# Performance work log

Measured on AMD Instinct MI355X. Metric: run time of the kernel, lower is better.

## Reference

```python
import jax, jax.numpy as jnp
import numpy as np

B, L, D = 4, 4096, 1024
H, M = 16, 256
DH = D // H  # 64


def setup_inputs() -> dict:
    key = jax.random.key(0)
    ks = jax.random.split(key, 7)
    s = 1.0 / np.sqrt(D).astype(np.float32)  # keep activations O(1) so exp() stays sane
    x = jax.random.normal(ks[0], (B, L, D), dtype=jnp.float32)
    Wq = jax.random.normal(ks[1], (D, D), dtype=jnp.float32) * s
    Wk = jax.random.normal(ks[2], (D, D), dtype=jnp.float32) * s
    Wv = jax.random.normal(ks[3], (D, D), dtype=jnp.float32) * s
    Wo = jax.random.normal(ks[4], (D, D), dtype=jnp.float32) * s
    bo = jnp.zeros((D,), dtype=jnp.float32)
    omega = jax.random.normal(ks[5], (DH, M), dtype=jnp.float32)
    return {"x": x, "Wq": Wq, "Wk": Wk, "Wv": Wv, "Wo": Wo, "bo": bo, "omega": omega}


def _phi(x, omega):
    # x: (B,H,L,dh) -> positive random features (B,H,L,m)
    scale = DH ** 0.25
    x_s = x / scale
    proj = jnp.einsum('bhld,dm->bhlm', x_s, omega)
    norm_sq = jnp.sum(x_s * x_s, axis=-1, keepdims=True) * 0.5
    return jnp.exp(proj - norm_sq) / (M ** 0.5)


def reference(x, Wq, Wk, Wv, Wo, bo, omega):
    # nn.Linear: y = x @ W.T
    def heads(W):
        return (x @ W.T).reshape(B, L, H, DH).transpose(0, 2, 1, 3)
    Q, K, V = heads(Wq), heads(Wk), heads(Wv)
    Q_feat = _phi(Q, omega)   # (B,H,L,m)
    K_feat = _phi(K, omega)   # (B,H,L,m)
    KV = jnp.einsum('bhlm,bhld->bhmd', K_feat, V)      # (B,H,m,dh)
    out = jnp.einsum('bhlm,bhmd->bhld', Q_feat, KV)    # (B,H,L,dh)
    K_sum = K_feat.sum(axis=2)                          # (B,H,m)
    norm = jnp.einsum('bhlm,bhm->bhl', Q_feat, K_sum)
    norm = jnp.clip(norm, 1e-6, None)[..., None]
    out = out / norm
    out = out.transpose(0, 2, 1, 3).reshape(B, L, D)
    return out @ Wo.T + bo
```

## Files before the change

### kernel.cpp

```cpp
#include <hip/hip_runtime.h>

typedef unsigned short u16;
typedef __attribute__((ext_vector_type(4))) float f32x4;
typedef _Float16 f16x8 __attribute__((ext_vector_type(8)));
typedef __attribute__((ext_vector_type(4))) u16   u16x4;
typedef __attribute__((ext_vector_type(8))) u16   u16x8;

#define DEV static __device__ __forceinline__

constexpr int Ll = 4096;

DEV float h2f(u16 v) { _Float16 h; __builtin_memcpy(&h, &v, 2); return (float)h; }
DEV u16 f2h(float f) { _Float16 h = (_Float16)f; u16 u; __builtin_memcpy(&u, &h, 2); return u; }

DEV f32x4 mfma16h(f16x8 a, f16x8 b, f32x4 c) {
    return __builtin_amdgcn_mfma_f32_16x16x32_f16(a, b, c, 0, 0, 0);
}

#if defined(__has_builtin)
#if __has_builtin(__builtin_amdgcn_global_load_lds)
#define HAS_GLLDS 1
#endif
#endif
#ifndef HAS_GLLDS
#define HAS_GLLDS 0
#endif

#if HAS_GLLDS
#define STAGE_T(DST, SRC, ROWBASE, KK)                                                    \
  { _Pragma("unroll") for (int j_ = 0; j_ < 2; j_++) {                                    \
      int row_ = wave * 32 + j_ * 16 + (lane >> 2);                                       \
      int col_ = ((lane & 3) ^ ((row_ >> 1) & 3)) * 8;                                    \
      const u16* gp_ = (SRC) + (size_t)((ROWBASE) + row_) * 1024 + (KK) + col_;           \
      __builtin_amdgcn_global_load_lds(                                                   \
          (const __attribute__((address_space(1))) unsigned int*)gp_,                     \
          (__attribute__((address_space(3))) unsigned int*)((DST) + (wave * 2 + j_) * 512), \
          16, 0, 0); } }
#else
#define STAGE_T(DST, SRC, ROWBASE, KK)                                                    \
  { int row_ = tid >> 1, cb_ = (tid & 1) * 16;                                            \
    const u16* gp_ = (SRC) + (size_t)((ROWBASE) + row_) * 1024 + (KK) + cb_;              \
    int g_ = ((row_ >> 1) & 3) << 3;                                                      \
    *(u16x8*)&(DST)[row_ * 32 + (cb_ ^ g_)]       = *(const u16x8*)gp_;                   \
    *(u16x8*)&(DST)[row_ * 32 + ((cb_ + 8) ^ g_)] = *(const u16x8*)(gp_ + 8); }
#endif

__global__ __launch_bounds__(256) void k_half(const float* __restrict__ s, u16* __restrict__ d) {
    size_t i = ((size_t)blockIdx.x * 256 + threadIdx.x) * 4;
    f32x4 v = *(const f32x4*)(s + i);
    u16x4 h;
#pragma unroll
    for (int j = 0; j < 4; j++) h[j] = f2h(v[j]);
    *(u16x4*)(d + i) = h;
}

__global__ __launch_bounds__(256) void k_omega(const float* __restrict__ om, u16* __restrict__ wh) {
    int i = blockIdx.x * 256 + threadIdx.x;
    int m = i >> 6, d = i & 63;
    wh[i] = f2h(om[d * 256 + m] * 0.35355339059327373f);
}

__global__ __launch_bounds__(256) void k_zero(float* __restrict__ p, int n) {
    int i = (blockIdx.x * 256 + threadIdx.x) * 4;
    if (i < n) { f32x4 z; z[0]=0.f; z[1]=0.f; z[2]=0.f; z[3]=0.f; *(f32x4*)(p + i) = z; }
}

__global__ __launch_bounds__(256) void k_gemm_qkv(
    const u16* __restrict__ Ax, const u16* __restrict__ Bw,
    u16* __restrict__ QK, u16* __restrict__ Vb) {
    __shared__ __align__(16) u16 sm[16384];
    const int tid = threadIdx.x, wave = tid >> 6, lane = tid & 63;
    const int lr = lane & 15, lk = (lane >> 4) * 8;
    const int m0 = blockIdx.y * 128, n0 = blockIdx.x * 128;
    const int wm = (wave >> 1) * 64, wn = (wave & 1) * 64;
    const int sec = n0 >> 10;
    constexpr int TILE = 4096, BUF = 8192;

    int aoff[4], boff[4];
#pragma unroll
    for (int f = 0; f < 4; f++) {
        int ra = wm + f * 16 + lr;
        aoff[f] = ra * 32 + (lk ^ (((ra >> 1) & 3) << 3));
        int rb = wn + f * 16 + lr;
        boff[f] = rb * 32 + (lk ^ (((rb >> 1) & 3) << 3));
    }

    f32x4 acc[4][4];
#pragma unroll
    for (int i = 0; i < 4; i++)
#pragma unroll
        for (int j = 0; j < 4; j++)
#pragma unroll
            for (int r = 0; r < 4; r++) acc[i][j][r] = 0.f;

    STAGE_T(sm, Ax, m0, 0)
    STAGE_T(sm + TILE, Bw, n0, 0)
    __syncthreads();

    int cur = 0;
    for (int k0 = 0; k0 < 1024; k0 += 32) {
        u16* buf  = sm + cur * BUF;
        u16* nbuf = sm + (cur ^ 1) * BUF;
        if (k0 + 32 < 1024) {
            STAGE_T(nbuf, Ax, m0, k0 + 32)
            STAGE_T(nbuf + TILE, Bw, n0, k0 + 32)
        }
        f16x8 a[4], bb[4];
#pragma unroll
        for (int f = 0; f < 4; f++) {
            a[f]  = *(const f16x8*)&buf[aoff[f]];
            bb[f] = *(const f16x8*)&buf[TILE + boff[f]];
        }
#pragma unroll
        for (int i = 0; i < 4; i++)
#pragma unroll
            for (int j = 0; j < 4; j++)
                acc[i][j] = mfma16h(a[i], bb[j], acc[i][j]);
        __syncthreads();
        cur ^= 1;
    }

    float* ep = (float*)sm;
    for (int g = 0; g < 4; g++) {
        __syncthreads();
        if ((wave >> 1) == (g >> 1)) {
#pragma unroll
            for (int fi = 0; fi < 2; fi++) {
                int fm = (g & 1) * 2 + fi;
#pragma unroll
                for (int j = 0; j < 4; j++)
#pragma unroll
                    for (int r = 0; r < 4; r++)
                        ep[(fi * 16 + (lane >> 4) * 4 + r) * 132 + wn + j * 16 + lr] = acc[fm][j][r];
            }
        }
        __syncthreads();
        int row = tid >> 3, c0 = (tid & 7) * 16;
        int grow = m0 + g * 32 + row;
        u16x8 h0, h1;
#pragma unroll
        for (int j = 0; j < 8; j++) {
            h0[j] = f2h(ep[row * 132 + c0 + j]);
            h1[j] = f2h(ep[row * 132 + c0 + 8 + j]);
        }
        if (sec < 2) {
            size_t o = (size_t)grow * 2048 + (n0 + c0);
            *(u16x8*)(QK + o) = h0; *(u16x8*)(QK + o + 8) = h1;
        } else {
            size_t o = (size_t)grow * 1024 + (n0 - 2048 + c0);
            *(u16x8*)(Vb + o) = h0; *(u16x8*)(Vb + o + 8) = h1;
        }
    }
}

__global__ __launch_bounds__(256) void k_phik_kv(
    const u16* __restrict__ QK, const u16* __restrict__ wt,
    const u16* __restrict__ Vb, float* __restrict__ KVacc, float* __restrict__ Ksum) {
    __shared__ __align__(16) u16 sKh[64 * 72];
    __shared__ __align__(16) u16 sVt[64 * 72];
    __shared__ __align__(16) u16 sKfT[256 * 72];
    __shared__ float snsq[64];
    const int tid = threadIdx.x, wave = tid >> 6, lane = tid & 63;
    const int lr = lane & 15, lk = (lane >> 4) * 8;
    const int kc = blockIdx.x, bh = blockIdx.y;
    const int b = bh >> 4, h = bh & 15;

    f16x8 wb[4][2];
#pragma unroll
    for (int fn = 0; fn < 4; fn++)
#pragma unroll
        for (int ks = 0; ks < 2; ks++)
            wb[fn][ks] = *(const f16x8*)(wt + (size_t)(wave * 64 + fn * 16 + lr) * 64 + ks * 32 + lk);

    f32x4 akv[4][4];
#pragma unroll
    for (int i = 0; i < 4; i++)
#pragma unroll
        for (int j = 0; j < 4; j++)
#pragma unroll
            for (int r = 0; r < 4; r++) akv[i][j][r] = 0.f;
    float ksm[4] = {0.f, 0.f, 0.f, 0.f};

    for (int it = 0; it < 8; it++) {
        int l0 = kc * 512 + it * 64;
        __syncthreads();
        {
            int row = tid >> 2, c0 = (tid & 3) * 16;
            size_t g = ((size_t)(b * Ll + l0 + row)) * 2048 + 1024 + h * 64 + c0;
            u16x8 h0 = *(const u16x8*)(QK + g);
            u16x8 h1 = *(const u16x8*)(QK + g + 8);
            *(u16x8*)&sKh[row * 72 + c0]     = h0;
            *(u16x8*)&sKh[row * 72 + c0 + 8] = h1;
            float s = 0.f;
#pragma unroll
            for (int j = 0; j < 8; j++) {
                float a = h2f(h0[j]); s += a * a;
                float c = h2f(h1[j]); s += c * c;
            }
            s += __shfl_xor(s, 1); s += __shfl_xor(s, 2);
            if ((tid & 3) == 0) snsq[row] = s * 0.0625f;
        }
        {
            int l = tid >> 2, d0 = (tid & 3) * 16;
            size_t g = ((size_t)(b * Ll + l0 + l)) * 1024 + h * 64 + d0;
            u16x8 v0 = *(const u16x8*)(Vb + g);
            u16x8 v1 = *(const u16x8*)(Vb + g + 8);
#pragma unroll
            for (int j = 0; j < 8; j++) {
                sVt[(d0 + j) * 72 + l] = v0[j];
                sVt[(d0 + 8 + j) * 72 + l] = v1[j];
            }
        }
        __syncthreads();
#pragma unroll
        for (int fm = 0; fm < 4; fm++) {
            f32x4 ap[4];
#pragma unroll
            for (int fn = 0; fn < 4; fn++)
#pragma unroll
                for (int r = 0; r < 4; r++) ap[fn][r] = 0.f;
#pragma unroll
            for (int ks = 0; ks < 2; ks++) {
                f16x8 aH = *(const f16x8*)&sKh[(fm * 16 + lr) * 72 + ks * 32 + lk];
#pragma unroll
                for (int fn = 0; fn < 4; fn++)
                    ap[fn] = mfma16h(aH, wb[fn][ks], ap[fn]);
            }
#pragma unroll
            for (int fn = 0; fn < 4; fn++) {
                u16x4 pk;
#pragma unroll
                for (int r = 0; r < 4; r++) {
                    float ns = snsq[fm * 16 + (lane >> 4) * 4 + r];
                    float val = __expf(ap[fn][r] - ns) * 0.00390625f;
                    ksm[fn] += val;
                    pk[r] = f2h(val);
                }
                *(u16x4*)&sKfT[(wave * 64 + fn * 16 + lr) * 72 + fm * 16 + (lane >> 4) * 4] = pk;
            }
        }
#pragma unroll
        for (int ks = 0; ks < 2; ks++) {
            f16x8 a4[4], b4[4];
#pragma unroll
            for (int f = 0; f < 4; f++) {
                a4[f] = *(const f16x8*)&sKfT[(wave * 64 + f * 16 + lr) * 72 + ks * 32 + lk];
                b4[f] = *(const f16x8*)&sVt[(f * 16 + lr) * 72 + ks * 32 + lk];
            }
#pragma unroll
            for (int fm = 0; fm < 4; fm++)
#pragma unroll
                for (int fn = 0; fn < 4; fn++)
                    akv[fm][fn] = mfma16h(a4[fm], b4[fn], akv[fm][fn]);
        }
    }
#pragma unroll
    for (int fm = 0; fm < 4; fm++)
#pragma unroll
        for (int fn = 0; fn < 4; fn++)
#pragma unroll
            for (int r = 0; r < 4; r++) {
                int m = wave * 64 + fm * 16 + (lane >> 4) * 4 + r;
                int d = fn * 16 + lr;
                atomicAdd(&KVacc[((size_t)bh << 14) + m * 64 + d], akv[fm][fn][r]);
            }
#pragma unroll
    for (int fn = 0; fn < 4; fn++) {
        ksm[fn] += __shfl_xor(ksm[fn], 16);
        ksm[fn] += __shfl_xor(ksm[fn], 32);
    }
    if (lane < 16) {
#pragma unroll
        for (int fn = 0; fn < 4; fn++)
            atomicAdd(&Ksum[bh * 256 + wave * 64 + fn * 16 + lane], ksm[fn]);
    }
}

__global__ __launch_bounds__(256) void k_kvt(const float* __restrict__ KVacc, u16* __restrict__ KVt) {
    int i = blockIdx.x * 256 + threadIdx.x;
    int bh = i >> 14, dd = (i >> 8) & 63, m = i & 255;
    KVt[i] = f2h(KVacc[((size_t)bh << 14) + m * 64 + dd]);
}

__global__ __launch_bounds__(512) void k_phiq_attn(
    const u16* __restrict__ QK, const u16* __restrict__ wt,
    const u16* __restrict__ KVt, const float* __restrict__ Ksum,
    u16* __restrict__ attn) {
    __shared__ __align__(16) u16 sQh[64 * 72];
    __shared__ __align__(16) u16 sQf[64 * 264];
    __shared__ float sKs[256];
    __shared__ float snsq[64];
    __shared__ float snorm[64];
    const int tid = threadIdx.x, wave = tid >> 6, lane = tid & 63;
    const int lr = lane & 15, lk = (lane >> 4) * 8;
    const int bh = blockIdx.y, b = bh >> 4, h = bh & 15;
    const int mq = wave & 3;
    const int lh = wave >> 2;
    const int af = wave & 3;
    const int ad = wave >> 2;

    f16x8 wb[4][2];
#pragma unroll
    for (int fn = 0; fn < 4; fn++)
#pragma unroll
        for (int ks = 0; ks < 2; ks++)
            wb[fn][ks] = *(const f16x8*)(wt + (size_t)(mq * 64 + fn * 16 + lr) * 64 + ks * 32 + lk);
    f16x8 kvb[2][8];
#pragma unroll
    for (int fn = 0; fn < 2; fn++)
#pragma unroll
        for (int ks = 0; ks < 8; ks++)
            kvb[fn][ks] = *(const f16x8*)(KVt + ((size_t)bh << 14) +
                                          (size_t)(ad * 32 + fn * 16 + lr) * 256 + ks * 32 + lk);
    if (tid < 256) sKs[tid] = Ksum[bh * 256 + tid];

    for (int st = 0; st < 2; st++) {
        const int l0 = (blockIdx.x * 2 + st) * 64;
        __syncthreads();
        {
            int row = tid >> 3, c0 = (tid & 7) * 8;
            size_t g = ((size_t)(b * Ll + l0 + row)) * 2048 + h * 64 + c0;
            u16x8 vh = *(const u16x8*)(QK + g);
            *(u16x8*)&sQh[row * 72 + c0] = vh;
            float s = 0.f;
#pragma unroll
            for (int j = 0; j < 8; j++) { float a = h2f(vh[j]); s += a * a; }
            s += __shfl_xor(s, 1); s += __shfl_xor(s, 2); s += __shfl_xor(s, 4);
            if ((tid & 7) == 0) snsq[row] = s * 0.0625f;
        }
        __syncthreads();
#pragma unroll
        for (int fm = 0; fm < 2; fm++) {
            f32x4 ap[4];
#pragma unroll
            for (int fn = 0; fn < 4; fn++)
#pragma unroll
                for (int r = 0; r < 4; r++) ap[fn][r] = 0.f;
#pragma unroll
            for (int ks = 0; ks < 2; ks++) {
                f16x8 aH = *(const f16x8*)&sQh[(lh * 32 + fm * 16 + lr) * 72 + ks * 32 + lk];
#pragma unroll
                for (int fn = 0; fn < 4; fn++)
                    ap[fn] = mfma16h(aH, wb[fn][ks], ap[fn]);
            }
#pragma unroll
            for (int fn = 0; fn < 4; fn++)
#pragma unroll
                for (int r = 0; r < 4; r++) {
                    int l = lh * 32 + fm * 16 + (lane >> 4) * 4 + r;
                    int m = mq * 64 + fn * 16 + lr;
                    sQf[l * 264 + m] = f2h(__expf(ap[fn][r] - snsq[l]) * 0.0625f);
                }
        }
        __syncthreads();
        {
            int l = tid >> 3, m0 = (tid & 7) * 32;
            float s = 0.f;
#pragma unroll
            for (int j = 0; j < 32; j++) s += h2f(sQf[l * 264 + m0 + j]) * sKs[m0 + j];
            s += __shfl_xor(s, 1); s += __shfl_xor(s, 2); s += __shfl_xor(s, 4);
            if ((tid & 7) == 0) snorm[l] = s;
        }
        f32x4 aa[2];
#pragma unroll
        for (int fn = 0; fn < 2; fn++)
#pragma unroll
            for (int r = 0; r < 4; r++) aa[fn][r] = 0.f;
#pragma unroll
        for (int ks = 0; ks < 8; ks++) {
            f16x8 a = *(const f16x8*)&sQf[(af * 16 + lr) * 264 + ks * 32 + lk];
            aa[0] = mfma16h(a, kvb[0][ks], aa[0]);
            aa[1] = mfma16h(a, kvb[1][ks], aa[1]);
        }
        __syncthreads();
        float* ep = (float*)sQf;
#pragma unroll
        for (int fn = 0; fn < 2; fn++)
#pragma unroll
            for (int r = 0; r < 4; r++) {
                int l = af * 16 + (lane >> 4) * 4 + r;
                int d = ad * 32 + fn * 16 + lr;
                ep[l * 68 + d] = aa[fn][r];
            }
        __syncthreads();
        {
            int l = tid >> 3, d0 = (tid & 7) * 8;
            float inv = 1.0f / fmaxf(snorm[l], 6.25e-8f);
            u16x8 o;
#pragma unroll
            for (int j = 0; j < 8; j++) o[j] = f2h(ep[l * 68 + d0 + j] * inv);
            *(u16x8*)(attn + ((size_t)(b * Ll + l0 + l)) * 1024 + h * 64 + d0) = o;
        }
    }
}

__global__ __launch_bounds__(256) void k_gemm_out(const u16* __restrict__ Ab, const u16* __restrict__ Bw,
                                                  const float* __restrict__ bias, float* __restrict__ outp) {
    __shared__ __align__(16) u16 sm[16896];
    const int tid = threadIdx.x, wave = tid >> 6, lane = tid & 63;
    const int lr = lane & 15, lk = (lane >> 4) * 8;
    const int m0 = blockIdx.y * 128, n0 = blockIdx.x * 128;
    const int wm = (wave >> 1) * 64, wn = (wave & 1) * 64;
    constexpr int TILE = 4096, BUF = 8192;

    int aoff[4], boff[4];
#pragma unroll
    for (int f = 0; f < 4; f++) {
        int ra = wm + f * 16 + lr;
        aoff[f] = ra * 32 + (lk ^ (((ra >> 1) & 3) << 3));
        int rb = wn + f * 16 + lr;
        boff[f] = rb * 32 + (lk ^ (((rb >> 1) & 3) << 3));
    }

    f32x4 acc[4][4];
#pragma unroll
    for (int i = 0; i < 4; i++)
#pragma unroll
        for (int j = 0; j < 4; j++)
#pragma unroll
            for (int r = 0; r < 4; r++) acc[i][j][r] = 0.f;

    STAGE_T(sm, Ab, m0, 0)
    STAGE_T(sm + TILE, Bw, n0, 0)
    __syncthreads();

    int cur = 0;
    for (int k0 = 0; k0 < 1024; k0 += 32) {
        u16* buf  = sm + cur * BUF;
        u16* nbuf = sm + (cur ^ 1) * BUF;
        if (k0 + 32 < 1024) {
            STAGE_T(nbuf, Ab, m0, k0 + 32)
            STAGE_T(nbuf + TILE, Bw, n0, k0 + 32)
        }
        f16x8 a[4], bb[4];
#pragma unroll
        for (int f = 0; f < 4; f++) {
            a[f]  = *(const f16x8*)&buf[aoff[f]];
            bb[f] = *(const f16x8*)&buf[TILE + boff[f]];
        }
#pragma unroll
        for (int i = 0; i < 4; i++)
#pragma unroll
            for (int j = 0; j < 4; j++)
                acc[i][j] = mfma16h(a[i], bb[j], acc[i][j]);
        __syncthreads();
        cur ^= 1;
    }
    float* ep = (float*)sm;
    for (int g = 0; g < 4; g++) {
        __syncthreads();
        if ((wave >> 1) == (g >> 1)) {
#pragma unroll
            for (int fi = 0; fi < 2; fi++) {
                int fm = (g & 1) * 2 + fi;
#pragma unroll
                for (int j = 0; j < 4; j++)
#pragma unroll
                    for (int r = 0; r < 4; r++)
                        ep[(fi * 16 + (lane >> 4) * 4 + r) * 132 + wn + j * 16 + lr] = acc[fm][j][r];
            }
        }
        __syncthreads();
        int row = tid >> 3, c0 = (tid & 7) * 16;
        int grow = m0 + g * 32 + row;
        float vv[16];
#pragma unroll
        for (int j = 0; j < 16; j++) vv[j] = ep[row * 132 + c0 + j] + bias[n0 + c0 + j];
#pragma unroll
        for (int p = 0; p < 4; p++) {
            f32x4 t;
#pragma unroll
            for (int q = 0; q < 4; q++) t[q] = vv[p * 4 + q];
            *(f32x4*)(outp + (size_t)grow * 1024 + n0 + c0 + p * 4) = t;
        }
    }
}

extern "C" void kernel_launch(void* const* d_in, const int* in_sizes, int n_in,
                              void* d_out, int out_size, void* d_ws, size_t ws_size,
                              hipStream_t stream) {
    (void)in_sizes; (void)n_in; (void)out_size; (void)ws_size;
    const float* x  = (const float*)d_in[0];
    const float* Wq = (const float*)d_in[1];
    const float* Wk = (const float*)d_in[2];
    const float* Wv = (const float*)d_in[3];
    const float* Wo = (const float*)d_in[4];
    const float* bo = (const float*)d_in[5];
    const float* om = (const float*)d_in[6];

    char* w = (char*)d_ws;
    size_t o = 0;
    auto take = [&](size_t n) { char* p = w + o; o += n; return p; };
    u16* QK  = (u16*)take(67108864);
    u16* Vb  = (u16*)take(33554432);
    u16* xh  = (u16*)take(33554432);
    u16* Wc  = (u16*)take(6291456);
    u16* Wof = (u16*)take(2097152);
    u16* wt  = (u16*)take(32768);
    float* KVacc = (float*)take(4194304);
    float* Ksum  = (float*)take(65536);
    u16* KVt = (u16*)take(2097152);
    u16* attn = Vb;

    k_half<<<16384, 256, 0, stream>>>(x, xh);
    k_half<<<1024, 256, 0, stream>>>(Wq, Wc);
    k_half<<<1024, 256, 0, stream>>>(Wk, Wc + 1048576);
    k_half<<<1024, 256, 0, stream>>>(Wv, Wc + 2097152);
    k_half<<<1024, 256, 0, stream>>>(Wo, Wof);
    k_omega<<<64, 256, 0, stream>>>(om, wt);
    k_zero<<<1040, 256, 0, stream>>>(KVacc, 1064960);

    k_gemm_qkv<<<dim3(24, 128), 256, 0, stream>>>(xh, Wc, QK, Vb);
    k_phik_kv<<<dim3(8, 64), 256, 0, stream>>>(QK, wt, Vb, KVacc, Ksum);
    k_kvt<<<4096, 256, 0, stream>>>(KVacc, KVt);
    k_phiq_attn<<<dim3(32, 64), 512, 0, stream>>>(QK, wt, KVt, Ksum, attn);
    k_gemm_out<<<dim3(8, 128), 256, 0, stream>>>(attn, Wof, bo, (float*)d_out);
}
```

Measured before the change: 410.4 us.

## Pipeline GEMM tiles with async LDS loads, split phi-K chunks, vectorize norm reads

Both GEMM kernels now keep two K-tiles of async global-to-LDS loads in flight. Each iteration waits on explicit vmcnt/lgkmcnt counters and barriers, then issues the next load into the buffer just consumed, so MFMA work overlaps memory latency. The phi-K/KV kernel splits the sequence into 16 chunks of 256 rows instead of 8 chunks of 512, doubling the grid for better occupancy at the cost of more atomic accumulation traffic. The Q normalizer dot product now reads the features from shared memory as 8-wide vectors instead of one element at a time. The hand-written waitcnt counts assume a fixed number of outstanding loads per STAGE_T, so the pipeline is only correct if that count holds.

```diff
diff --git a/kernel.cpp b/kernel.cpp
--- a/kernel.cpp
+++ b/kernel.cpp
@@ -93,10 +93,45 @@
 #pragma unroll
             for (int r = 0; r < 4; r++) acc[i][j][r] = 0.f;
 
+#if HAS_GLLDS
+    STAGE_T(sm,              Ax, m0, 0)
+    STAGE_T(sm + TILE,       Bw, n0, 0)
+    STAGE_T(sm + BUF,        Ax, m0, 32)
+    STAGE_T(sm + BUF + TILE, Bw, n0, 32)
+    int cur = 0;
+    for (int t = 0; t < 32; ++t) {
+        if (t < 31) { asm volatile("s_waitcnt vmcnt(4)" ::: "memory"); }
+        else        { asm volatile("s_waitcnt vmcnt(0)" ::: "memory"); }
+        __builtin_amdgcn_sched_barrier(0);
+        __builtin_amdgcn_s_barrier();
+        __builtin_amdgcn_sched_barrier(0);
+        u16* buf = sm + cur * BUF;
+        f16x8 a[4], bb[4];
+#pragma unroll
+        for (int f = 0; f < 4; f++) {
+            a[f]  = *(const f16x8*)&buf[aoff[f]];
+            bb[f] = *(const f16x8*)&buf[TILE + boff[f]];
+        }
+        asm volatile("s_waitcnt lgkmcnt(0)" ::: "memory");
+        __builtin_amdgcn_sched_barrier(0);
+        __builtin_amdgcn_s_barrier();
+        __builtin_amdgcn_sched_barrier(0);
+        if (t < 30) {
+            int kk = (t + 2) * 32;
+            STAGE_T(buf,        Ax, m0, kk)
+            STAGE_T(buf + TILE, Bw, n0, kk)
+        }
+#pragma unroll
+        for (int i = 0; i < 4; i++)
+#pragma unroll
+            for (int j = 0; j < 4; j++)
+                acc[i][j] = mfma16h(a[i], bb[j], acc[i][j]);
+        cur ^= 1;
+    }
+#else
     STAGE_T(sm, Ax, m0, 0)
     STAGE_T(sm + TILE, Bw, n0, 0)
     __syncthreads();
-
     int cur = 0;
     for (int k0 = 0; k0 < 1024; k0 += 32) {
         u16* buf  = sm + cur * BUF;
@@ -119,6 +154,7 @@
         __syncthreads();
         cur ^= 1;
     }
+#endif
 
     float* ep = (float*)sm;
     for (int g = 0; g < 4; g++) {
@@ -181,8 +217,8 @@
             for (int r = 0; r < 4; r++) akv[i][j][r] = 0.f;
     float ksm[4] = {0.f, 0.f, 0.f, 0.f};
 
-    for (int it = 0; it < 8; it++) {
-        int l0 = kc * 512 + it * 64;
+    for (int it = 0; it < 4; it++) {
+        int l0 = kc * 256 + it * 64;
         __syncthreads();
         {
             int row = tid >> 2, c0 = (tid & 3) * 16;
@@ -357,7 +393,11 @@
             int l = tid >> 3, m0 = (tid & 7) * 32;
             float s = 0.f;
 #pragma unroll
-            for (int j = 0; j < 32; j++) s += h2f(sQf[l * 264 + m0 + j]) * sKs[m0 + j];
+            for (int j4 = 0; j4 < 4; j4++) {
+                u16x8 qv = *(const u16x8*)&sQf[l * 264 + m0 + j4 * 8];
+#pragma unroll
+                for (int j = 0; j < 8; j++) s += h2f(qv[j]) * sKs[m0 + j4 * 8 + j];
+            }
             s += __shfl_xor(s, 1); s += __shfl_xor(s, 2); s += __shfl_xor(s, 4);
             if ((tid & 7) == 0) snorm[l] = s;
         }
@@ -420,10 +460,45 @@
 #pragma unroll
             for (int r = 0; r < 4; r++) acc[i][j][r] = 0.f;
 
+#if HAS_GLLDS
+    STAGE_T(sm,              Ab, m0, 0)
+    STAGE_T(sm + TILE,       Bw, n0, 0)
+    STAGE_T(sm + BUF,        Ab, m0, 32)
+    STAGE_T(sm + BUF + TILE, Bw, n0, 32)
+    int cur = 0;
+    for (int t = 0; t < 32; ++t) {
+        if (t < 31) { asm volatile("s_waitcnt vmcnt(4)" ::: "memory"); }
+        else        { asm volatile("s_waitcnt vmcnt(0)" ::: "memory"); }
+        __builtin_amdgcn_sched_barrier(0);
+        __builtin_amdgcn_s_barrier();
+        __builtin_amdgcn_sched_barrier(0);
+        u16* buf = sm + cur * BUF;
+        f16x8 a[4], bb[4];
+#pragma unroll
+        for (int f = 0; f < 4; f++) {
+            a[f]  = *(const f16x8*)&buf[aoff[f]];
+            bb[f] = *(const f16x8*)&buf[TILE + boff[f]];
+        }
+        asm volatile("s_waitcnt lgkmcnt(0)" ::: "memory");
+        __builtin_amdgcn_sched_barrier(0);
+        __builtin_amdgcn_s_barrier();
+        __builtin_amdgcn_sched_barrier(0);
+        if (t < 30) {
+            int kk = (t + 2) * 32;
+            STAGE_T(buf,        Ab, m0, kk)
+            STAGE_T(buf + TILE, Bw, n0, kk)
+        }
+#pragma unroll
+        for (int i = 0; i < 4; i++)
+#pragma unroll
+            for (int j = 0; j < 4; j++)
+                acc[i][j] = mfma16h(a[i], bb[j], acc[i][j]);
+        cur ^= 1;
+    }
+#else
     STAGE_T(sm, Ab, m0, 0)
     STAGE_T(sm + TILE, Bw, n0, 0)
     __syncthreads();
-
     int cur = 0;
     for (int k0 = 0; k0 < 1024; k0 += 32) {
         u16* buf  = sm + cur * BUF;
@@ -446,6 +521,7 @@
         __syncthreads();
         cur ^= 1;
     }
+#endif
     float* ep = (float*)sm;
     for (int g = 0; g < 4; g++) {
         __syncthreads();
@@ -511,7 +587,7 @@
     k_zero<<<1040, 256, 0, stream>>>(KVacc, 1064960);
 
     k_gemm_qkv<<<dim3(24, 128), 256, 0, stream>>>(xh, Wc, QK, Vb);
-    k_phik_kv<<<dim3(8, 64), 256, 0, stream>>>(QK, wt, Vb, KVacc, Ksum);
+    k_phik_kv<<<dim3(16, 64), 256, 0, stream>>>(QK, wt, Vb, KVacc, Ksum);
     k_kvt<<<4096, 256, 0, stream>>>(KVacc, KVt);
     k_phiq_attn<<<dim3(32, 64), 512, 0, stream>>>(QK, wt, KVt, Ksum, attn);
     k_gemm_out<<<dim3(8, 128), 256, 0, stream>>>(attn, Wof, bo, (float*)d_out);
```

Measured after the change: 413.0 us. No clear change (+0.6%).

## Enlarge QKV and output GEMM tiles to 256x256 with interleaved barrier schedule

Applied to the files above, without the earlier changes.

Rewrites both projection GEMMs to use 512-thread blocks computing 256x256 tiles, with each wave owning a 128x64 sub-tile. The K loop is split into two MFMA halves separated by explicit s_barrier, waitcnt and setprio calls, so global-to-LDS prefetch of the next stage overlaps compute. This raises operand reuse per LDS byte and cuts the total block count. It also doubles the phi(K)·V split along L to 16 chunks for more parallelism, and vectorises the Q-norm dot-product reads from LDS. The costs are higher register and LDS use per block and more atomic accumulation traffic in the KV stage.

```diff
diff --git a/kernel.cpp b/kernel.cpp
--- a/kernel.cpp
+++ b/kernel.cpp
@@ -27,22 +27,25 @@
 #endif
 
 #if HAS_GLLDS
-#define STAGE_T(DST, SRC, ROWBASE, KK)                                                    \
-  { _Pragma("unroll") for (int j_ = 0; j_ < 2; j_++) {                                    \
-      int row_ = wave * 32 + j_ * 16 + (lane >> 2);                                       \
-      int col_ = ((lane & 3) ^ ((row_ >> 1) & 3)) * 8;                                    \
-      const u16* gp_ = (SRC) + (size_t)((ROWBASE) + row_) * 1024 + (KK) + col_;           \
-      __builtin_amdgcn_global_load_lds(                                                   \
-          (const __attribute__((address_space(1))) unsigned int*)gp_,                     \
-          (__attribute__((address_space(3))) unsigned int*)((DST) + (wave * 2 + j_) * 512), \
-          16, 0, 0); } }
+#define STG(BUF, U, SRC, ROWBASE, KK)                                                \
+  { int rl_ = wave * 16 + (lane >> 2);                                               \
+    int c_ = lane & 3;                                                               \
+    int grow_ = (((U) & 1) * 128) + rl_;                                             \
+    const u16* gp_ = (SRC) + (size_t)((ROWBASE) + grow_) * 1024 + (KK)               \
+                     + ((c_ ^ ((rl_ >> 1) & 3)) * 8);                                \
+    __builtin_amdgcn_global_load_lds(                                                \
+        (const __attribute__((address_space(1))) unsigned int*)gp_,                  \
+        (__attribute__((address_space(3))) unsigned int*)(sm + (BUF) * 16384 +       \
+            (U) * 4096 + wave * 512), 16, 0, 0); }
 #else
-#define STAGE_T(DST, SRC, ROWBASE, KK)                                                    \
-  { int row_ = tid >> 1, cb_ = (tid & 1) * 16;                                            \
-    const u16* gp_ = (SRC) + (size_t)((ROWBASE) + row_) * 1024 + (KK) + cb_;              \
-    int g_ = ((row_ >> 1) & 3) << 3;                                                      \
-    *(u16x8*)&(DST)[row_ * 32 + (cb_ ^ g_)]       = *(const u16x8*)gp_;                   \
-    *(u16x8*)&(DST)[row_ * 32 + ((cb_ + 8) ^ g_)] = *(const u16x8*)(gp_ + 8); }
+#define STG(BUF, U, SRC, ROWBASE, KK)                                                \
+  { int rl_ = wave * 16 + (lane >> 2);                                               \
+    int c_ = lane & 3;                                                               \
+    int grow_ = (((U) & 1) * 128) + rl_;                                             \
+    const u16* gp_ = (SRC) + (size_t)((ROWBASE) + grow_) * 1024 + (KK)               \
+                     + ((c_ ^ ((rl_ >> 1) & 3)) * 8);                                \
+    *(u16x8*)(sm + (BUF) * 16384 + (U) * 4096 + wave * 512 + lane * 8)               \
+        = *(const u16x8*)gp_; }
 #endif
 
 __global__ __launch_bounds__(256) void k_half(const float* __restrict__ s, u16* __restrict__ d) {
@@ -65,83 +68,113 @@
     if (i < n) { f32x4 z; z[0]=0.f; z[1]=0.f; z[2]=0.f; z[3]=0.f; *(f32x4*)(p + i) = z; }
 }
 
-__global__ __launch_bounds__(256) void k_gemm_qkv(
+__global__ __launch_bounds__(512, 2) void k_gemm_qkv(
     const u16* __restrict__ Ax, const u16* __restrict__ Bw,
     u16* __restrict__ QK, u16* __restrict__ Vb) {
-    __shared__ __align__(16) u16 sm[16384];
+    __shared__ __align__(16) u16 sm[32768];
     const int tid = threadIdx.x, wave = tid >> 6, lane = tid & 63;
-    const int lr = lane & 15, lk = (lane >> 4) * 8;
-    const int m0 = blockIdx.y * 128, n0 = blockIdx.x * 128;
-    const int wm = (wave >> 1) * 64, wn = (wave & 1) * 64;
+    const int lr = lane & 15, lkq = lane >> 4;
+    const int wr = wave >> 2, wc = wave & 3;
+    const int m0 = blockIdx.y * 256, n0 = blockIdx.x * 256;
     const int sec = n0 >> 10;
-    constexpr int TILE = 4096, BUF = 8192;
-
-    int aoff[4], boff[4];
+
+    int aoff[8], boff[4];
+#pragma unroll
+    for (int f = 0; f < 8; f++) {
+        int row = wr * 128 + f * 16 + lr;
+        aoff[f] = row * 32 + ((lkq ^ ((row >> 1) & 3)) * 8);
+    }
 #pragma unroll
     for (int f = 0; f < 4; f++) {
-        int ra = wm + f * 16 + lr;
-        aoff[f] = ra * 32 + (lk ^ (((ra >> 1) & 3) << 3));
-        int rb = wn + f * 16 + lr;
-        boff[f] = rb * 32 + (lk ^ (((rb >> 1) & 3) << 3));
-    }
-
-    f32x4 acc[4][4];
-#pragma unroll
-    for (int i = 0; i < 4; i++)
+        int row = wc * 64 + f * 16 + lr;
+        boff[f] = row * 32 + ((lkq ^ ((row >> 1) & 3)) * 8);
+    }
+
+    f32x4 acc[8][4];
+#pragma unroll
+    for (int i = 0; i < 8; i++)
 #pragma unroll
         for (int j = 0; j < 4; j++)
 #pragma unroll
             for (int r = 0; r < 4; r++) acc[i][j][r] = 0.f;
 
-    STAGE_T(sm, Ax, m0, 0)
-    STAGE_T(sm + TILE, Bw, n0, 0)
-    __syncthreads();
-
-    int cur = 0;
-    for (int k0 = 0; k0 < 1024; k0 += 32) {
-        u16* buf  = sm + cur * BUF;
-        u16* nbuf = sm + (cur ^ 1) * BUF;
-        if (k0 + 32 < 1024) {
-            STAGE_T(nbuf, Ax, m0, k0 + 32)
-            STAGE_T(nbuf + TILE, Bw, n0, k0 + 32)
-        }
-        f16x8 a[4], bb[4];
-#pragma unroll
-        for (int f = 0; f < 4; f++) {
-            a[f]  = *(const f16x8*)&buf[aoff[f]];
-            bb[f] = *(const f16x8*)&buf[TILE + boff[f]];
-        }
+    STG(0, 0, Ax, m0, 0) STG(0, 1, Ax, m0, 0)
+    STG(0, 2, Bw, n0, 0) STG(0, 3, Bw, n0, 0)
+    asm volatile("s_waitcnt vmcnt(0)" ::: "memory");
+    __builtin_amdgcn_sched_barrier(0);
+    __builtin_amdgcn_s_barrier();
+    __builtin_amdgcn_sched_barrier(0);
+
+    int cb = 0;
+    for (int t = 0; t < 32; ++t) {
+        const u16* Abase = sm + cb * 16384;
+        const u16* Bbase = Abase + 8192;
+        f16x8 afr[4], bfr[4];
+#pragma unroll
+        for (int f = 0; f < 4; f++) bfr[f] = *(const f16x8*)&Bbase[boff[f]];
+#pragma unroll
+        for (int f = 0; f < 4; f++) afr[f] = *(const f16x8*)&Abase[aoff[f]];
+        if (t < 31) {
+            int kk = (t + 1) * 32;
+            STG(cb ^ 1, 0, Ax, m0, kk) STG(cb ^ 1, 1, Ax, m0, kk)
+            STG(cb ^ 1, 2, Bw, n0, kk) STG(cb ^ 1, 3, Bw, n0, kk)
+        }
+        __builtin_amdgcn_sched_barrier(0);
+        __builtin_amdgcn_s_barrier();
+        asm volatile("s_waitcnt lgkmcnt(0)" ::: "memory");
+        __builtin_amdgcn_sched_barrier(0);
+        __builtin_amdgcn_s_setprio(1);
 #pragma unroll
         for (int i = 0; i < 4; i++)
 #pragma unroll
             for (int j = 0; j < 4; j++)
-                acc[i][j] = mfma16h(a[i], bb[j], acc[i][j]);
-        __syncthreads();
-        cur ^= 1;
+                acc[i][j] = mfma16h(afr[i], bfr[j], acc[i][j]);
+        __builtin_amdgcn_s_setprio(0);
+        __builtin_amdgcn_sched_barrier(0);
+        __builtin_amdgcn_s_barrier();
+        __builtin_amdgcn_sched_barrier(0);
+#pragma unroll
+        for (int f = 0; f < 4; f++) afr[f] = *(const f16x8*)&Abase[aoff[4 + f]];
+        __builtin_amdgcn_sched_barrier(0);
+        __builtin_amdgcn_s_barrier();
+        asm volatile("s_waitcnt lgkmcnt(0)" ::: "memory");
+        __builtin_amdgcn_sched_barrier(0);
+        __builtin_amdgcn_s_setprio(1);
+#pragma unroll
+        for (int i = 0; i < 4; i++)
+#pragma unroll
+            for (int j = 0; j < 4; j++)
+                acc[4 + i][j] = mfma16h(afr[i], bfr[j], acc[4 + i][j]);
+        __builtin_amdgcn_s_setprio(0);
+        asm volatile("s_waitcnt vmcnt(0)" ::: "memory");
+        __builtin_amdgcn_sched_barrier(0);
+        __builtin_amdgcn_s_barrier();
+        __builtin_amdgcn_sched_barrier(0);
+        cb ^= 1;
     }
 
     float* ep = (float*)sm;
-    for (int g = 0; g < 4; g++) {
-        __syncthreads();
-        if ((wave >> 1) == (g >> 1)) {
+    for (int g = 0; g < 8; g++) {
+        __syncthreads();
+        if (wr == (g >> 2)) {
 #pragma unroll
             for (int fi = 0; fi < 2; fi++) {
-                int fm = (g & 1) * 2 + fi;
-#pragma unroll
-                for (int j = 0; j < 4; j++)
+                int fm = (g & 3) * 2 + fi;
+#pragma unroll
+                for (int fn = 0; fn < 4; fn++)
 #pragma unroll
                     for (int r = 0; r < 4; r++)
-                        ep[(fi * 16 + (lane >> 4) * 4 + r) * 132 + wn + j * 16 + lr] = acc[fm][j][r];
-            }
-        }
-        __syncthreads();
-        int row = tid >> 3, c0 = (tid & 7) * 16;
+                        ep[(fi * 16 + (lane >> 4) * 4 + r) * 264 + wc * 64 + fn * 16 + lr] = acc[fm][fn][r];
+            }
+        }
+        __syncthreads();
+        int row = tid >> 4, c0 = (tid & 15) * 16;
         int grow = m0 + g * 32 + row;
         u16x8 h0, h1;
 #pragma unroll
         for (int j = 0; j < 8; j++) {
-            h0[j] = f2h(ep[row * 132 + c0 + j]);
-            h1[j] = f2h(ep[row * 132 + c0 + 8 + j]);
+            h0[j] = f2h(ep[row * 264 + c0 + j]);
+            h1[j] = f2h(ep[row * 264 + c0 + 8 + j]);
         }
         if (sec < 2) {
             size_t o = (size_t)grow * 2048 + (n0 + c0);
@@ -149,6 +182,120 @@
         } else {
             size_t o = (size_t)grow * 1024 + (n0 - 2048 + c0);
             *(u16x8*)(Vb + o) = h0; *(u16x8*)(Vb + o + 8) = h1;
+        }
+    }
+}
+
+__global__ __launch_bounds__(512, 2) void k_gemm_out(
+    const u16* __restrict__ Ab, const u16* __restrict__ Bw,
+    const float* __restrict__ bias, float* __restrict__ outp) {
+    __shared__ __align__(16) u16 sm[32768];
+    const int tid = threadIdx.x, wave = tid >> 6, lane = tid & 63;
+    const int lr = lane & 15, lkq = lane >> 4;
+    const int wr = wave >> 2, wc = wave & 3;
+    const int m0 = blockIdx.y * 256, n0 = blockIdx.x * 256;
+
+    int aoff[8], boff[4];
+#pragma unroll
+    for (int f = 0; f < 8; f++) {
+        int row = wr * 128 + f * 16 + lr;
+        aoff[f] = row * 32 + ((lkq ^ ((row >> 1) & 3)) * 8);
+    }
+#pragma unroll
+    for (int f = 0; f < 4; f++) {
+        int row = wc * 64 + f * 16 + lr;
+        boff[f] = row * 32 + ((lkq ^ ((row >> 1) & 3)) * 8);
+    }
+
+    f32x4 acc[8][4];
+#pragma unroll
+    for (int i = 0; i < 8; i++)
+#pragma unroll
+        for (int j = 0; j < 4; j++)
+#pragma unroll
+            for (int r = 0; r < 4; r++) acc[i][j][r] = 0.f;
+
+    STG(0, 0, Ab, m0, 0) STG(0, 1, Ab, m0, 0)
+    STG(0, 2, Bw, n0, 0) STG(0, 3, Bw, n0, 0)
+    asm volatile("s_waitcnt vmcnt(0)" ::: "memory");
+    __builtin_amdgcn_sched_barrier(0);
+    __builtin_amdgcn_s_barrier();
+    __builtin_amdgcn_sched_barrier(0);
+
+    int cb = 0;
+    for (int t = 0; t < 32; ++t) {
+        const u16* Abase = sm + cb * 16384;
+        const u16* Bbase = Abase + 8192;
+        f16x8 afr[4], bfr[4];
+#pragma unroll
+        for (int f = 0; f < 4; f++) bfr[f] = *(const f16x8*)&Bbase[boff[f]];
+#pragma unroll
+        for (int f = 0; f < 4; f++) afr[f] = *(const f16x8*)&Abase[aoff[f]];
+        if (t < 31) {
+            int kk = (t + 1) * 32;
+            STG(cb ^ 1, 0, Ab, m0, kk) STG(cb ^ 1, 1, Ab, m0, kk)
+            STG(cb ^ 1, 2, Bw, n0, kk) STG(cb ^ 1, 3, Bw, n0, kk)
+        }
+        __builtin_amdgcn_sched_barrier(0);
+        __builtin_amdgcn_s_barrier();
+        asm volatile("s_waitcnt lgkmcnt(0)" ::: "memory");
+        __builtin_amdgcn_sched_barrier(0);
+        __builtin_amdgcn_s_setprio(1);
+#pragma unroll
+        for (int i = 0; i < 4; i++)
+#pragma unroll
+            for (int j = 0; j < 4; j++)
+                acc[i][j] = mfma16h(afr[i], bfr[j], acc[i][j]);
+        __builtin_amdgcn_s_setprio(0);
+        __builtin_amdgcn_sched_barrier(0);
+        __builtin_amdgcn_s_barrier();
+        __builtin_amdgcn_sched_barrier(0);
+#pragma unroll
+        for (int f = 0; f < 4; f++) afr[f] = *(const f16x8*)&Abase[aoff[4 + f]];
+        __builtin_amdgcn_sched_barrier(0);
+        __builtin_amdgcn_s_barrier();
+        asm volatile("s_waitcnt lgkmcnt(0)" ::: "memory");
+        __builtin_amdgcn_sched_barrier(0);
+        __builtin_amdgcn_s_setprio(1);
+#pragma unroll
+        for (int i = 0; i < 4; i++)
+#pragma unroll
+            for (int j = 0; j < 4; j++)
+                acc[4 + i][j] = mfma16h(afr[i], bfr[j], acc[4 + i][j]);
+        __builtin_amdgcn_s_setprio(0);
+        asm volatile("s_waitcnt vmcnt(0)" ::: "memory");
+        __builtin_amdgcn_sched_barrier(0);
+        __builtin_amdgcn_s_barrier();
+        __builtin_amdgcn_sched_barrier(0);
+        cb ^= 1;
+    }
+
+    float* ep = (float*)sm;
+    for (int g = 0; g < 8; g++) {
+        __syncthreads();
+        if (wr == (g >> 2)) {
+#pragma unroll
+            for (int fi = 0; fi < 2; fi++) {
+                int fm = (g & 3) * 2 + fi;
+#pragma unroll
+                for (int fn = 0; fn < 4; fn++)
+#pragma unroll
+                    for (int r = 0; r < 4; r++)
+                        ep[(fi * 16 + (lane >> 4) * 4 + r) * 264 + wc * 64 + fn * 16 + lr] = acc[fm][fn][r];
+            }
+        }
+        __syncthreads();
+        int row = tid >> 4, c0 = (tid & 15) * 16;
+        int grow = m0 + g * 32 + row;
+        float vv[16];
+#pragma unroll
+        for (int j = 0; j < 16; j++) vv[j] = ep[row * 264 + c0 + j] + bias[n0 + c0 + j];
+#pragma unroll
+        for (int p = 0; p < 4; p++) {
+            f32x4 tv;
+#pragma unroll
+            for (int q = 0; q < 4; q++) tv[q] = vv[p * 4 + q];
+            *(f32x4*)(outp + (size_t)grow * 1024 + n0 + c0 + p * 4) = tv;
         }
     }
 }
@@ -181,8 +328,8 @@
             for (int r = 0; r < 4; r++) akv[i][j][r] = 0.f;
     float ksm[4] = {0.f, 0.f, 0.f, 0.f};
 
-    for (int it = 0; it < 8; it++) {
-        int l0 = kc * 512 + it * 64;
+    for (int it = 0; it < 4; it++) {
+        int l0 = kc * 256 + it * 64;
         __syncthreads();
         {
             int row = tid >> 2, c0 = (tid & 3) * 16;
@@ -357,7 +504,11 @@
             int l = tid >> 3, m0 = (tid & 7) * 32;
             float s = 0.f;
 #pragma unroll
-            for (int j = 0; j < 32; j++) s += h2f(sQf[l * 264 + m0 + j]) * sKs[m0 + j];
+            for (int j4 = 0; j4 < 4; j4++) {
+                u16x8 qv = *(const u16x8*)&sQf[l * 264 + m0 + j4 * 8];
+#pragma unroll
+                for (int j = 0; j < 8; j++) s += h2f(qv[j]) * sKs[m0 + j4 * 8 + j];
+            }
             s += __shfl_xor(s, 1); s += __shfl_xor(s, 2); s += __shfl_xor(s, 4);
             if ((tid & 7) == 0) snorm[l] = s;
         }
@@ -390,88 +541,6 @@
 #pragma unroll
             for (int j = 0; j < 8; j++) o[j] = f2h(ep[l * 68 + d0 + j] * inv);
             *(u16x8*)(attn + ((size_t)(b * Ll + l0 + l)) * 1024 + h * 64 + d0) = o;
-        }
-    }
-}
-
-__global__ __launch_bounds__(256) void k_gemm_out(const u16* __restrict__ Ab, const u16* __restrict__ Bw,
-                                                  const float* __restrict__ bias, float* __restrict__ outp) {
-    __shared__ __align__(16) u16 sm[16896];
-    const int tid = threadIdx.x, wave = tid >> 6, lane = tid & 63;
-    const int lr = lane & 15, lk = (lane >> 4) * 8;
-    const int m0 = blockIdx.y * 128, n0 = blockIdx.x * 128;
-    const int wm = (wave >> 1) * 64, wn = (wave & 1) * 64;
-    constexpr int TILE = 4096, BUF = 8192;
-
-    int aoff[4], boff[4];
-#pragma unroll
-    for (int f = 0; f < 4; f++) {
-        int ra = wm + f * 16 + lr;
-        aoff[f] = ra * 32 + (lk ^ (((ra >> 1) & 3) << 3));
-        int rb = wn + f * 16 + lr;
-        boff[f] = rb * 32 + (lk ^ (((rb >> 1) & 3) << 3));
-    }
-
-    f32x4 acc[4][4];
-#pragma unroll
-    for (int i = 0; i < 4; i++)
-#pragma unroll
-        for (int j = 0; j < 4; j++)
-#pragma unroll
-            for (int r = 0; r < 4; r++) acc[i][j][r] = 0.f;
-
-    STAGE_T(sm, Ab, m0, 0)
-    STAGE_T(sm + TILE, Bw, n0, 0)
-    __syncthreads();
-
-    int cur = 0;
-    for (int k0 = 0; k0 < 1024; k0 += 32) {
-        u16* buf  = sm + cur * BUF;
-        u16* nbuf = sm + (cur ^ 1) * BUF;
-        if (k0 + 32 < 1024) {
-            STAGE_T(nbuf, Ab, m0, k0 + 32)
-            STAGE_T(nbuf + TILE, Bw, n0, k0 + 32)
-        }
-        f16x8 a[4], bb[4];
-#pragma unroll
-        for (int f = 0; f < 4; f++) {
-            a[f]  = *(const f16x8*)&buf[aoff[f]];
-            bb[f] = *(const f16x8*)&buf[TILE + boff[f]];
-        }
-#pragma unroll
-        for (int i = 0; i < 4; i++)
-#pragma unroll
-            for (int j = 0; j < 4; j++)
-                acc[i][j] = mfma16h(a[i], bb[j], acc[i][j]);
-        __syncthreads();
-        cur ^= 1;
-    }
-    float* ep = (float*)sm;
-    for (int g = 0; g < 4; g++) {
-        __syncthreads();
-        if ((wave >> 1) == (g >> 1)) {
-#pragma unroll
-            for (int fi = 0; fi < 2; fi++) {
-                int fm = (g & 1) * 2 + fi;
-#pragma unroll
-                for (int j = 0; j < 4; j++)
-#pragma unroll
-                    for (int r = 0; r < 4; r++)
-                        ep[(fi * 16 + (lane >> 4) * 4 + r) * 132 + wn + j * 16 + lr] = acc[fm][j][r];
-            }
-        }
-        __syncthreads();
-        int row = tid >> 3, c0 = (tid & 7) * 16;
-        int grow = m0 + g * 32 + row;
-        float vv[16];
-#pragma unroll
-        for (int j = 0; j < 16; j++) vv[j] = ep[row * 132 + c0 + j] + bias[n0 + c0 + j];
-#pragma unroll
-        for (int p = 0; p < 4; p++) {
-            f32x4 t;
-#pragma unroll
-            for (int q = 0; q < 4; q++) t[q] = vv[p * 4 + q];
-            *(f32x4*)(outp + (size_t)grow * 1024 + n0 + c0 + p * 4) = t;
         }
     }
 }
@@ -510,9 +579,9 @@
     k_omega<<<64, 256, 0, stream>>>(om, wt);
     k_zero<<<1040, 256, 0, stream>>>(KVacc, 1064960);
 
-    k_gemm_qkv<<<dim3(24, 128), 256, 0, stream>>>(xh, Wc, QK, Vb);
-    k_phik_kv<<<dim3(8, 64), 256, 0, stream>>>(QK, wt, Vb, KVacc, Ksum);
+    k_gemm_qkv<<<dim3(12, 64), 512, 0, stream>>>(xh, Wc, QK, Vb);
+    k_phik_kv<<<dim3(16, 64), 256, 0, stream>>>(QK, wt, Vb, KVacc, Ksum);
     k_kvt<<<4096, 256, 0, stream>>>(KVacc, KVt);
     k_phiq_attn<<<dim3(32, 64), 512, 0, stream>>>(QK, wt, KVt, Ksum, attn);
-    k_gemm_out<<<dim3(8, 128), 256, 0, stream>>>(attn, Wof, bo, (float*)d_out);
-}
+    k_gemm_out<<<dim3(4, 64), 512, 0, stream>>>(attn, Wof, bo, (float*)d_out);
+}
```

After: 412.3 us. About the same (+0.4%).
